# Optimization experiments

Hardware: AMD Instinct MI355X
Metric: run time of the kernel (lower is better)

Reference implementation:

```python
import jax, jax.numpy as jnp
import numpy as np

N = 8192  # number of nodes (input_size[0])
K = 32    # number of archetypes


def setup_inputs() -> dict:
    key = jax.random.key(0)
    kA, kb, ka, kX, kC = jax.random.split(key, 5)
    A = (jax.random.uniform(kA, (N, N)) < 0.05).astype(jnp.float32)
    beta = jax.random.normal(kb, (N,), dtype=jnp.float32)
    a = jax.random.normal(ka, (1,), dtype=jnp.float32)
    X = jax.random.normal(kX, (K, N), dtype=jnp.float32)
    C = jax.random.normal(kC, (N, K), dtype=jnp.float32)
    return {"A": A, "beta": beta, "a": a, "X": X, "C": C}


def reference(A, beta, a, X, C):
    # z_dist[i,j] = (X[:,i]-X[:,j])^T C_s^T K C_s (X[:,i]-X[:,j]),
    # with K = softmax(X)^T softmax(X), C_s = softmax(C) (both column-softmax, dim=0).
    Xs = jax.nn.softmax(X, axis=0)          # (K, N)
    Cs = jax.nn.softmax(C, axis=0)          # (N, K)
    E = Xs @ Cs                             # (K, K) = softmax(X) @ softmax(C)
    M = E.T @ E                             # (K, K) = Cs^T Xs^T Xs Cs, PSD
    # quadratic form over all pairs via G = X^T M X (raw X columns, as in the torch loop)
    G = X.T @ (M @ X)                       # (N, N)
    q = jnp.diagonal(G)                     # (N,) = x_i^T M x_i
    z_dist = q[:, None] + q[None, :] - 2.0 * G
    theta = beta[:, None] + beta[None, :] - a * z_dist  # (N, N)
    sp = jax.nn.softplus(theta)
    LL = 0.5 * jnp.sum(theta * A) - 0.5 * (jnp.sum(sp) - jnp.sum(jnp.diagonal(sp)))
    return LL
```

## Files before the change

kernel.cpp:

```cpp
#include <hip/hip_runtime.h>
#include <hip/hip_bf16.h>

#define NN 8192
#define KK 32

typedef __attribute__((ext_vector_type(8))) short short8v;
typedef __attribute__((ext_vector_type(4))) float float4v;

__device__ __forceinline__ float wave_reduce_sum(float v) {
    #pragma unroll
    for (int off = 32; off > 0; off >>= 1) v += __shfl_down(v, off);
    return v;
}
__device__ __forceinline__ unsigned short f2bf(float x) {
    unsigned int u = __float_as_uint(x);
    return (unsigned short)((u + 0x7fffu + ((u >> 16) & 1u)) >> 16);
}

__global__ __launch_bounds__(256) void kE(const float* __restrict__ X,
                                          const float* __restrict__ C,
                                          float* __restrict__ Ep,
                                          float* __restrict__ sC) {
    __shared__ float xe[KK * 33];
    __shared__ float ce[32 * 33];
    __shared__ float xs[32];
    const int tid = threadIdx.x;
    const int r = tid >> 5, q = tid & 31;
    const int nb = blockIdx.x * 32;
    #pragma unroll
    for (int u = 0; u < 4; ++u) {
        xe[(r + 8 * u) * 33 + q] = __expf(X[(size_t)(r + 8 * u) * NN + nb + q]);
        ce[(r + 8 * u) * 33 + q] = __expf(C[(size_t)(nb + r + 8 * u) * KK + q]);
    }
    __syncthreads();
    if (tid < 32) {
        float s = 0.f;
        #pragma unroll
        for (int k = 0; k < 32; ++k) s += xe[k * 33 + tid];
        xs[tid] = 1.f / s;
    } else if (tid < 64) {
        const int l = tid - 32;
        float s = 0.f;
        #pragma unroll
        for (int n = 0; n < 32; ++n) s += ce[n * 33 + l];
        atomicAdd(&sC[l], s);
    }
    __syncthreads();
    #pragma unroll
    for (int u = 0; u < 4; ++u) {
        const int k = r + 8 * u;
        float acc = 0.f;
        #pragma unroll
        for (int n = 0; n < 32; ++n)
            acc = fmaf(xe[k * 33 + n] * xs[n], ce[n * 33 + q], acc);
        atomicAdd(&Ep[k * KK + q], acc);
    }
}

__global__ __launch_bounds__(256) void kp_prep(
    const float* __restrict__ X, const float* __restrict__ beta,
    const float* __restrict__ a_ptr, const float* __restrict__ Ep,
    const float* __restrict__ sC,
    float* __restrict__ f, unsigned short* __restrict__ Xh,
    unsigned short* __restrict__ Wh, double* __restrict__ acc) {
    __shared__ float el[KK * 33];
    __shared__ float rs[32];
    __shared__ float Ml[KK * KK];
    const int tid = threadIdx.x;
    const int r = tid >> 5, q = tid & 31;
    #pragma unroll
    for (int u = 0; u < 4; ++u)
        el[(r + 8 * u) * 33 + q] = Ep[(r + 8 * u) * KK + q];
    if (tid < 32) rs[tid] = 1.f / sC[tid];
    __syncthreads();
    #pragma unroll
    for (int u = 0; u < 4; ++u) {
        const int l1 = r + 8 * u;
        float m = 0.f;
        #pragma unroll
        for (int k = 0; k < KK; ++k)
            m = fmaf(el[k * 33 + l1], el[k * 33 + q], m);
        Ml[l1 * KK + q] = m * rs[l1] * rs[q];
    }
    __syncthreads();

    const int n = blockIdx.x * 256 + tid;
    float x[KK], v[KK];
    #pragma unroll
    for (int k = 0; k < KK; ++k) x[k] = X[(size_t)k * NN + n];
    const float a = a_ptr[0];
    const float two_a = 2.f * a;
    #pragma unroll
    for (int l = 0; l < KK; ++l) {
        float s = 0.f;
        #pragma unroll
        for (int k = 0; k < KK; ++k) s = fmaf(Ml[l * KK + k], x[k], s);
        v[l] = two_a * s;
    }
    float q2 = 0.f;
    #pragma unroll
    for (int l = 0; l < KK; ++l) q2 = fmaf(x[l], v[l], q2);
    const float b = beta[n];
    const float fn = b - 0.5f * q2;
    f[n] = fn;

    union PK { unsigned short u[8]; short8v s; };
    PK xh, wh;
    #pragma unroll
    for (int g = 0; g < 4; ++g) {
        #pragma unroll
        for (int e = 0; e < 8; ++e) {
            const int k = g * 8 + e;
            xh.u[e] = f2bf(x[k]);
            wh.u[e] = f2bf(v[k]);
        }
        *(short8v*)&Xh[(size_t)n * KK + g * 8] = xh.s;
        *(short8v*)&Wh[(size_t)n * KK + g * 8] = wh.s;
    }
    const float th = 2.f * b;
    float sp = fmaxf(th, 0.f) + __logf(1.f + __expf(-fabsf(th)));
    sp = wave_reduce_sum(sp);
    if ((tid & 63) == 0) atomicAdd(&acc[2], (double)sp);
}

__global__ __launch_bounds__(256, 6) void k_pair(
    const float* __restrict__ A, const float* __restrict__ f,
    const unsigned short* __restrict__ Xh, const unsigned short* __restrict__ Wh,
    float* __restrict__ part) {
    const int tid  = threadIdx.x;
    const int lane = tid & 63;
    const int l15  = lane & 15;
    const int klo  = (lane >> 4) << 3;
    const int r0   = (lane >> 4) << 2;
    const int wid  = blockIdx.x * 4 + (tid >> 6);
    const int ibase = (wid >> 5) << 5;
    const int jc    = (wid & 31) << 8;

    const short8v xh0 = *(const short8v*)&Xh[(size_t)(ibase + l15) * KK + klo];
    const short8v xh1 = *(const short8v*)&Xh[(size_t)(ibase + 16 + l15) * KK + klo];
    float fr[2][4];
    #pragma unroll
    for (int s = 0; s < 2; ++s)
        #pragma unroll
        for (int r = 0; r < 4; ++r) fr[s][r] = f[ibase + 16 * s + r0 + r];

    float accA = 0.f, accS = 0.f;
    #pragma unroll 2
    for (int jt = 0; jt < 16; ++jt) {
        const int jb = jc + (jt << 4);
        const short8v wf = *(const short8v*)&Wh[(size_t)(jb + l15) * KK + klo];
        const float fj = f[jb + l15];
        #pragma unroll
        for (int s = 0; s < 2; ++s) {
            float av[4];
            #pragma unroll
            for (int r = 0; r < 4; ++r)
                av[r] = A[(size_t)(ibase + 16 * s + r0 + r) * NN + jb + l15];
            float4v d = {0.f, 0.f, 0.f, 0.f};
            d = __builtin_amdgcn_mfma_f32_16x16x32_bf16(s ? xh1 : xh0, wf, d, 0, 0, 0);
            #pragma unroll
            for (int r = 0; r < 4; ++r) {
                const float th = fr[s][r] + fj + d[r];
                accA = fmaf(th, av[r], accA);
                accS += fmaxf(th, 0.f) + __logf(1.f + __expf(-fabsf(th)));
            }
        }
    }

    accA = wave_reduce_sum(accA);
    accS = wave_reduce_sum(accS);
    __shared__ float rA[4], rS[4];
    if (lane == 0) { rA[tid >> 6] = accA; rS[tid >> 6] = accS; }
    __syncthreads();
    if (tid == 0) {
        part[blockIdx.x * 2]     = rA[0] + rA[1] + rA[2] + rA[3];
        part[blockIdx.x * 2 + 1] = rS[0] + rS[1] + rS[2] + rS[3];
    }
}

__global__ __launch_bounds__(1024) void kz_final(const float* __restrict__ part,
                                                 const double* __restrict__ acc,
                                                 float* __restrict__ out) {
    const int t = threadIdx.x;
    double dA = (double)part[2 * t]     + (double)part[2 * (t + 1024)];
    double dS = (double)part[2 * t + 1] + (double)part[2 * (t + 1024) + 1];
    #pragma unroll
    for (int off = 32; off > 0; off >>= 1) {
        dA += __shfl_down(dA, off);
        dS += __shfl_down(dS, off);
    }
    __shared__ double sA[16], sS[16];
    if ((t & 63) == 0) { sA[t >> 6] = dA; sS[t >> 6] = dS; }
    __syncthreads();
    if (t == 0) {
        double a = 0.0, s = 0.0;
        #pragma unroll
        for (int u = 0; u < 16; ++u) { a += sA[u]; s += sS[u]; }
        out[0] = (float)(0.5 * (a - (s - acc[2])));
    }
}

extern "C" void kernel_launch(void* const* d_in, const int* in_sizes, int n_in,
                              void* d_out, int out_size, void* d_ws, size_t ws_size,
                              hipStream_t stream) {
    const float* Ain    = (const float*)d_in[0];
    const float* betain = (const float*)d_in[1];
    const float* ain    = (const float*)d_in[2];
    const float* Xin    = (const float*)d_in[3];
    const float* Cin    = (const float*)d_in[4];
    float* out = (float*)d_out;

    char* ws = (char*)d_ws;
    float*          Ep    = (float*)(ws + 0);
    double*         acc   = (double*)(ws + 4096);
    float*          sC    = (float*)(ws + 4224);
    float*          f     = (float*)(ws + 8704);
    float*          part  = (float*)(ws + 49152);
    unsigned short* Xh    = (unsigned short*)(ws + 65536);
    unsigned short* Wh    = (unsigned short*)(ws + 589824);

    hipMemsetAsync(ws, 0, 4352, stream);

    kE<<<256, 256, 0, stream>>>(Xin, Cin, Ep, sC);
    kp_prep<<<NN / 256, 256, 0, stream>>>(Xin, betain, ain, Ep, sC, f, Xh, Wh, acc);
    k_pair<<<2048, 256, 0, stream>>>(Ain, f, Xh, Wh, part);
    kz_final<<<1, 1024, 0, stream>>>(part, acc, out);
}
```

Before: 409.7 us.

## Pack binary adjacency into bitmasks before the pairwise kernel

Adds a k_pack pass that reads A once with coalesced float4 loads and uses wave ballots to store it as 64-bit bitmasks. k_pair then reads one small bitmask per row segment instead of scattered 64-byte float strips of A, and extracts each A value by shift and mask. The MFMA operands are swapped so each lane's output rows match the bit layout, and f_j is loaded as a float4. This moves the A bandwidth cost into a separate streaming kernel and adds an extra launch and workspace traffic. It also assumes A holds only 0/1 values, so any nonzero entry becomes 1.

```diff
diff --git a/kernel.cpp b/kernel.cpp
--- a/kernel.cpp
+++ b/kernel.cpp
@@ -15,6 +15,26 @@
 __device__ __forceinline__ unsigned short f2bf(float x) {
     unsigned int u = __float_as_uint(x);
     return (unsigned short)((u + 0x7fffu + ((u >> 16) & 1u)) >> 16);
+}
+
+__global__ __launch_bounds__(256) void k_pack(const float* __restrict__ A,
+                                              unsigned long long* __restrict__ Abits) {
+    const int lane = threadIdx.x & 63;
+    const int row  = blockIdx.x * 4 + (threadIdx.x >> 6);
+    const float* ar = &A[(size_t)row * NN];
+    #pragma unroll 2
+    for (int it = 0; it < 32; ++it) {
+        const float4 a = *(const float4*)&ar[it * 256 + lane * 4];
+        const unsigned long long b0 = __ballot(a.x != 0.f);
+        const unsigned long long b1 = __ballot(a.y != 0.f);
+        const unsigned long long b2 = __ballot(a.z != 0.f);
+        const unsigned long long b3 = __ballot(a.w != 0.f);
+        if (lane < 4) {
+            const unsigned long long v =
+                (lane == 0) ? b0 : (lane == 1) ? b1 : (lane == 2) ? b2 : b3;
+            Abits[((size_t)row * 32 + it) * 4 + lane] = v;
+        }
+    }
 }
 
 __global__ __launch_bounds__(256) void kE(const float* __restrict__ X,
@@ -124,45 +144,69 @@
 }
 
 __global__ __launch_bounds__(256, 6) void k_pair(
-    const float* __restrict__ A, const float* __restrict__ f,
+    const unsigned long long* __restrict__ Abits, const float* __restrict__ f,
     const unsigned short* __restrict__ Xh, const unsigned short* __restrict__ Wh,
     float* __restrict__ part) {
     const int tid  = threadIdx.x;
     const int lane = tid & 63;
     const int l15  = lane & 15;
-    const int klo  = (lane >> 4) << 3;
-    const int r0   = (lane >> 4) << 2;
+    const int g4   = lane >> 4;
+    const int klo  = g4 << 3;
+    const int r0   = g4 << 2;
     const int wid  = blockIdx.x * 4 + (tid >> 6);
     const int ibase = (wid >> 5) << 5;
     const int jc    = (wid & 31) << 8;
+    const int seg   = jc >> 8;
 
     const short8v xh0 = *(const short8v*)&Xh[(size_t)(ibase + l15) * KK + klo];
     const short8v xh1 = *(const short8v*)&Xh[(size_t)(ibase + 16 + l15) * KK + klo];
-    float fr[2][4];
-    #pragma unroll
-    for (int s = 0; s < 2; ++s)
-        #pragma unroll
-        for (int r = 0; r < 4; ++r) fr[s][r] = f[ibase + 16 * s + r0 + r];
+    const float fi0 = f[ibase + l15];
+    const float fi1 = f[ibase + 16 + l15];
+
+    const ulonglong2* p0 =
+        (const ulonglong2*)&Abits[((size_t)(ibase + l15) * 32 + seg) * 4];
+    const ulonglong2* p1 =
+        (const ulonglong2*)&Abits[((size_t)(ibase + 16 + l15) * 32 + seg) * 4];
+    const ulonglong2 q00 = p0[0], q01 = p0[1];
+    const ulonglong2 q10 = p1[0], q11 = p1[1];
+    const unsigned lo0[4] = {(unsigned)q00.x, (unsigned)q00.y,
+                             (unsigned)q01.x, (unsigned)q01.y};
+    const unsigned hi0[4] = {(unsigned)(q00.x >> 32), (unsigned)(q00.y >> 32),
+                             (unsigned)(q01.x >> 32), (unsigned)(q01.y >> 32)};
+    const unsigned lo1[4] = {(unsigned)q10.x, (unsigned)q10.y,
+                             (unsigned)q11.x, (unsigned)q11.y};
+    const unsigned hi1[4] = {(unsigned)(q10.x >> 32), (unsigned)(q10.y >> 32),
+                             (unsigned)(q11.x >> 32), (unsigned)(q11.y >> 32)};
 
     float accA = 0.f, accS = 0.f;
-    #pragma unroll 2
-    for (int jt = 0; jt < 16; ++jt) {
-        const int jb = jc + (jt << 4);
-        const short8v wf = *(const short8v*)&Wh[(size_t)(jb + l15) * KK + klo];
-        const float fj = f[jb + l15];
-        #pragma unroll
-        for (int s = 0; s < 2; ++s) {
-            float av[4];
-            #pragma unroll
-            for (int r = 0; r < 4; ++r)
-                av[r] = A[(size_t)(ibase + 16 * s + r0 + r) * NN + jb + l15];
-            float4v d = {0.f, 0.f, 0.f, 0.f};
-            d = __builtin_amdgcn_mfma_f32_16x16x32_bf16(s ? xh1 : xh0, wf, d, 0, 0, 0);
+    for (int half = 0; half < 2; ++half) {
+        unsigned c0[4], c1[4];
+        #pragma unroll
+        for (int r = 0; r < 4; ++r) {
+            c0[r] = half ? hi0[r] : lo0[r];
+            c1[r] = half ? hi1[r] : lo1[r];
+        }
+        #pragma unroll 2
+        for (int jt2 = 0; jt2 < 8; ++jt2) {
+            const int jb = jc + (((half << 3) + jt2) << 4);
+            const unsigned sh = (unsigned)(jt2 << 2) + (unsigned)g4;
+            const short8v wf = *(const short8v*)&Wh[(size_t)(jb + l15) * KK + klo];
+            const float4 fj = *(const float4*)&f[jb + r0];
+            float4v d0 = {0.f, 0.f, 0.f, 0.f};
+            float4v d1 = {0.f, 0.f, 0.f, 0.f};
+            d0 = __builtin_amdgcn_mfma_f32_16x16x32_bf16(wf, xh0, d0, 0, 0, 0);
+            d1 = __builtin_amdgcn_mfma_f32_16x16x32_bf16(wf, xh1, d1, 0, 0, 0);
+            const float* fjp = (const float*)&fj;
             #pragma unroll
             for (int r = 0; r < 4; ++r) {
-                const float th = fr[s][r] + fj + d[r];
-                accA = fmaf(th, av[r], accA);
-                accS += fmaxf(th, 0.f) + __logf(1.f + __expf(-fabsf(th)));
+                const float av0 = (float)((c0[r] >> sh) & 1u);
+                const float av1 = (float)((c1[r] >> sh) & 1u);
+                const float th0 = fi0 + fjp[r] + d0[r];
+                const float th1 = fi1 + fjp[r] + d1[r];
+                accA = fmaf(th0, av0, accA);
+                accA = fmaf(th1, av1, accA);
+                accS += fmaxf(th0, 0.f) + __logf(1.f + __expf(-fabsf(th0)));
+                accS += fmaxf(th1, 0.f) + __logf(1.f + __expf(-fabsf(th1)));
             }
         }
     }
@@ -211,18 +255,20 @@
     float* out = (float*)d_out;
 
     char* ws = (char*)d_ws;
-    float*          Ep    = (float*)(ws + 0);
-    double*         acc   = (double*)(ws + 4096);
-    float*          sC    = (float*)(ws + 4224);
-    float*          f     = (float*)(ws + 8704);
-    float*          part  = (float*)(ws + 49152);
-    unsigned short* Xh    = (unsigned short*)(ws + 65536);
-    unsigned short* Wh    = (unsigned short*)(ws + 589824);
+    float*              Ep    = (float*)(ws + 0);
+    double*             acc   = (double*)(ws + 4096);
+    float*              sC    = (float*)(ws + 4224);
+    float*              f     = (float*)(ws + 8704);
+    float*              part  = (float*)(ws + 49152);
+    unsigned short*     Xh    = (unsigned short*)(ws + 65536);
+    unsigned short*     Wh    = (unsigned short*)(ws + 589824);
+    unsigned long long* Abits = (unsigned long long*)(ws + 1114112);
 
     hipMemsetAsync(ws, 0, 4352, stream);
 
+    k_pack<<<2048, 256, 0, stream>>>(Ain, Abits);
     kE<<<256, 256, 0, stream>>>(Xin, Cin, Ep, sC);
     kp_prep<<<NN / 256, 256, 0, stream>>>(Xin, betain, ain, Ep, sC, f, Xh, Wh, acc);
-    k_pair<<<2048, 256, 0, stream>>>(Ain, f, Xh, Wh, part);
+    k_pair<<<2048, 256, 0, stream>>>(Abits, f, Xh, Wh, part);
     kz_final<<<1, 1024, 0, stream>>>(part, acc, out);
 }
```

After: 436.1 us. 6.4% more time.
